# Kernel optimization log

Hardware: AMD Instinct MI355X
Metric: run time of the kernel (lower is better)

## Reference

```python
import jax, jax.numpy as jnp
import numpy as np

N, D, E, H, K = 16384, 1024, 16, 4096, 2


def setup_inputs() -> dict:
    key = jax.random.key(0)
    ks = jax.random.split(key, 6)
    s = 0.02
    return {
        "x": jax.random.normal(ks[0], (N, D), jnp.float32),
        "Wr": jax.random.normal(ks[1], (D, E), jnp.float32) * s,
        "br": jnp.zeros((E,), jnp.float32),
        "Wn": jax.random.normal(ks[2], (D, E), jnp.float32) * s,
        "bn": jnp.zeros((E,), jnp.float32),
        "W1": jax.random.normal(ks[3], (E, D, H), jnp.float32) * s,
        "b1": jnp.zeros((E, H), jnp.float32),
        "W2": jax.random.normal(ks[4], (E, H, 1), jnp.float32) * s,
        "b2": jnp.zeros((E, 1), jnp.float32),
        "k": K,
    }


def reference(x, Wr, br, Wn, bn, W1, b1, W2, b2, k):
    # Router. NOTE: faithful to source — top-k and scattered values come from
    # noise_logits; logits/noise feed only noisy_logits which is dead (only used
    # as a shape template for the -inf tensor), so the randn noise is omitted.
    noise_logits = x @ Wn + bn                      # [N, E]
    vals, idx = jax.lax.top_k(noise_logits, k)      # [N, k]
    # softmax over sparse(-inf filled) logits == softmax over top-k values,
    # scattered back; non-selected experts get exactly 0.
    probs = jax.nn.softmax(vals, axis=-1)           # [N, k]
    n = x.shape[0]
    gates = jnp.zeros((n, noise_logits.shape[-1]), x.dtype)
    gates = gates.at[jnp.arange(n)[:, None], idx].set(probs)  # [N, E]

    # Dense loop over ALL experts (as in source), masked-weighted sum.
    def step(acc, per_expert):
        w1, bb1, w2, bb2, g = per_expert
        h = jax.nn.relu(x @ w1 + bb1)               # [N, H]
        out = h @ w2 + bb2                          # [N, 1]
        return acc + out * g[:, None], None

    init = jnp.zeros((n, 1), x.dtype)
    final_out, _ = jax.lax.scan(step, init, (W1, b1, W2, b2, gates.T))
    return final_out
```

## Files before the change

kernel.cpp:

```cpp
#include <hip/hip_runtime.h>
#include <stdint.h>

#define N_TOK 16384
#define DIM   1024
#define NEXP  16
#define HID   4096

typedef unsigned short ushort_t;
typedef __bf16 bf16x8 __attribute__((ext_vector_type(8)));
typedef float  f32x4  __attribute__((ext_vector_type(4)));
typedef ushort_t u16x8 __attribute__((ext_vector_type(8)));

__device__ __forceinline__ ushort_t f2bf(float f) {
    union { float f; unsigned int u; } v; v.f = f;
    unsigned int r = v.u + 0x7fffu + ((v.u >> 16) & 1u);
    return (ushort_t)(r >> 16);
}

__device__ __forceinline__ void gl_lds16(const void* g, void* l) {
    __builtin_amdgcn_global_load_lds(
        (const __attribute__((address_space(1))) void*)g,
        (__attribute__((address_space(3))) void*)l, 16, 0, 0);
}

#define TS 72
__global__ void __launch_bounds__(256) transpose_w1_kernel(const float* __restrict__ W1,
                                                           ushort_t* __restrict__ w1t) {
    __shared__ ushort_t tileT[64 * TS];
    const int e  = blockIdx.z;
    const int h0 = blockIdx.x * 256;
    const int d0 = blockIdx.y * 64;
    const int t  = threadIdx.x;
    const int hs = t & 15;
    const int dg = t >> 4;
    const float* src = W1 + (size_t)e * DIM * HID;
    float4 rows[4][4];
#pragma unroll
    for (int i = 0; i < 4; ++i) {
        const float* rp = src + (size_t)(d0 + dg * 4 + i) * HID + h0 + hs * 4;
#pragma unroll
        for (int ii = 0; ii < 4; ++ii)
            rows[ii][i] = *(const float4*)(rp + ii * 64);
    }
    ushort_t* dst = w1t + (size_t)e * HID * DIM;
#pragma unroll
    for (int ii = 0; ii < 4; ++ii) {
        if (ii) __syncthreads();
#pragma unroll
        for (int j = 0; j < 4; ++j) {
            float v0 = (&rows[ii][0].x)[j], v1 = (&rows[ii][1].x)[j];
            float v2 = (&rows[ii][2].x)[j], v3 = (&rows[ii][3].x)[j];
            ushort4 col; col.x = f2bf(v0); col.y = f2bf(v1); col.z = f2bf(v2); col.w = f2bf(v3);
            *(ushort4*)&tileT[(hs * 4 + j) * TS + dg * 4] = col;
        }
        __syncthreads();
#pragma unroll
        for (int p = 0; p < 2; ++p) {
            int r = p * 32 + (t >> 3);
            int c = t & 7;
            u16x8 fr = *(const u16x8*)&tileT[r * TS + c * 8];
            *(u16x8*)(dst + (size_t)(h0 + ii * 64 + r) * DIM + d0 + c * 8) = fr;
        }
    }
}

__global__ void __launch_bounds__(256) router_logits_kernel(
    const float* __restrict__ x, const float* __restrict__ Wn,
    const float* __restrict__ bn, const float* __restrict__ b2,
    ushort_t* __restrict__ xbf, int2* __restrict__ eidx,
    float2* __restrict__ probs, float* __restrict__ out) {
    int wave  = threadIdx.x >> 6;
    int lane  = threadIdx.x & 63;
    int token = blockIdx.x * 4 + wave;
    const float* xr = x + (size_t)token * DIM;
    float acc[NEXP];
#pragma unroll
    for (int e = 0; e < NEXP; ++e) acc[e] = 0.f;
    ushort_t xl[16];
#pragma unroll
    for (int i = 0; i < 16; ++i) {
        int d = lane + i * 64;
        float xv = xr[d];
        xl[i] = f2bf(xv);
        const float4* wr = (const float4*)(Wn + d * NEXP);
        float4 w0 = wr[0], w1 = wr[1], w2 = wr[2], w3 = wr[3];
        acc[0]  += xv * w0.x; acc[1]  += xv * w0.y; acc[2]  += xv * w0.z; acc[3]  += xv * w0.w;
        acc[4]  += xv * w1.x; acc[5]  += xv * w1.y; acc[6]  += xv * w1.z; acc[7]  += xv * w1.w;
        acc[8]  += xv * w2.x; acc[9]  += xv * w2.y; acc[10] += xv * w2.z; acc[11] += xv * w2.w;
        acc[12] += xv * w3.x; acc[13] += xv * w3.y; acc[14] += xv * w3.z; acc[15] += xv * w3.w;
    }
    ushort_t* xbr = xbf + (size_t)token * DIM;
#pragma unroll
    for (int i = 0; i < 16; ++i) xbr[lane + i * 64] = xl[i];
#pragma unroll
    for (int e = 0; e < NEXP; ++e) {
        float v = acc[e];
#pragma unroll
        for (int off = 32; off > 0; off >>= 1) v += __shfl_xor(v, off, 64);
        acc[e] = v + bn[e];
    }
    if (lane == 0) {
        float m0 = -1e30f; int i0 = 0;
        for (int e = 0; e < NEXP; ++e) if (acc[e] > m0) { m0 = acc[e]; i0 = e; }
        float m1 = -1e30f; int i1 = 0;
        for (int e = 0; e < NEXP; ++e) if (e != i0 && acc[e] > m1) { m1 = acc[e]; i1 = e; }
        float tq = expf(m1 - m0);
        float p0 = 1.f / (1.f + tq);
        float p1 = 1.f - p0;
        eidx[token]  = make_int2(i0, i1);
        probs[token] = make_float2(p0, p1);
        out[token]   = p0 * b2[i0] + p1 * b2[i1];
    }
}

#define NCHUNK 64
#define CHUNK  (N_TOK / NCHUNK)

__global__ void __launch_bounds__(256) hist_kernel(const int2* __restrict__ eidx,
                                                   int* __restrict__ counts) {
    __shared__ int h[NEXP];
    const int t = threadIdx.x;
    if (t < NEXP) h[t] = 0;
    __syncthreads();
    int token = blockIdx.x * CHUNK + t;
    int2 ei = eidx[token];
    atomicAdd(&h[ei.x], 1);
    atomicAdd(&h[ei.y], 1);
    __syncthreads();
    if (t < NEXP) counts[t * NCHUNK + blockIdx.x] = h[t];
}

__global__ void __launch_bounds__(1024) scan_kernel(const int* __restrict__ counts,
                                                    int* __restrict__ offs,
                                                    int* __restrict__ cnt) {
    const int w    = threadIdx.x >> 6;
    const int lane = threadIdx.x & 63;
    int v = counts[w * NCHUNK + lane];
    int orig = v;
#pragma unroll
    for (int off = 1; off < 64; off <<= 1) {
        int up = __shfl_up(v, off, 64);
        if (lane >= off) v += up;
    }
    offs[w * NCHUNK + lane] = v - orig;
    if (lane == 63) cnt[w] = v;
}

__global__ void __launch_bounds__(256) scatter_kernel(
    const int2* __restrict__ eidx, const float2* __restrict__ probs,
    const int* __restrict__ offs, int* __restrict__ tok, float* __restrict__ gate) {
    __shared__ int wcnt[4][NEXP];
    const int t = threadIdx.x;
    const int wv = t >> 6, lane = t & 63;
    const int token = blockIdx.x * CHUNK + t;
    int2  ei = eidx[token];
    float2 pr = probs[token];
    unsigned long long lmask = (1ull << lane) - 1ull;
#pragma unroll
    for (int e = 0; e < NEXP; ++e) {
        bool s = (ei.x == e) | (ei.y == e);
        unsigned long long m = __ballot(s);
        if (lane == 0) wcnt[wv][e] = __popcll(m);
    }
    __syncthreads();
#pragma unroll
    for (int e = 0; e < NEXP; ++e) {
        bool s0 = (ei.x == e);
        bool s  = s0 | (ei.y == e);
        unsigned long long m = __ballot(s);
        int base = offs[e * NCHUNK + blockIdx.x];
        for (int w = 0; w < wv; ++w) base += wcnt[w][e];
        int pos = base + __popcll(m & lmask);
        if (s) {
            tok[e * N_TOK + pos]  = token;
            gate[e * N_TOK + pos] = s0 ? pr.x : pr.y;
        }
    }
}

__global__ void __launch_bounds__(256, 2) moe_ffn_kernel(
    const ushort_t* __restrict__ xbf, const ushort_t* __restrict__ w1t,
    const float* __restrict__ b1, const float* __restrict__ w2,
    const int* __restrict__ tok, const float* __restrict__ gate,
    const int* __restrict__ cnt, float* __restrict__ out, int eoff) {
    __shared__ ushort_t Alds[128 * 64];
    __shared__ ushort_t Blds[128 * 64];
    const int e  = blockIdx.z + eoff;
    const int ce = cnt[e];
    const int m0 = blockIdx.y * 128;
    if (m0 >= ce) return;
    const int h0 = blockIdx.x * 128;
    const int t    = threadIdx.x;
    const int wv   = t >> 6;
    const int lane = t & 63;
    const int quad = lane >> 4;
    const int ln   = lane & 15;
    const int wm   = (wv >> 1) * 64;
    const int wn   = (wv & 1) * 64;

    int tkid[4];
#pragma unroll
    for (int i = 0; i < 4; ++i) {
        int f = i * 256 + t;
        int r = f >> 3;
        int rr = (m0 + r < ce) ? (m0 + r) : m0;
        tkid[i] = tok[e * N_TOK + rr];
    }

    f32x4 acc[4][4];
    const f32x4 zero = {0.f, 0.f, 0.f, 0.f};
#pragma unroll
    for (int mi = 0; mi < 4; ++mi)
#pragma unroll
        for (int ni = 0; ni < 4; ++ni) acc[mi][ni] = zero;

    for (int k0 = 0; k0 < DIM; k0 += 64) {
#pragma unroll
        for (int i = 0; i < 4; ++i) {
            int f = i * 256 + t;
            int r = f >> 3, c = f & 7;
            int cs = (c ^ (r & 7)) << 3;
            const ushort_t* ga = xbf + (size_t)tkid[i] * DIM + k0 + cs;
            gl_lds16(ga, &Alds[f * 8]);
            const ushort_t* gb = w1t + ((size_t)e * HID + h0 + r) * DIM + k0 + cs;
            gl_lds16(gb, &Blds[f * 8]);
        }
        __syncthreads();
#pragma unroll
        for (int ks = 0; ks < 2; ++ks) {
            int q = ks * 4 + quad;
            int csw = (q ^ (ln & 7)) << 3;
            bf16x8 af[4], bfr[4];
#pragma unroll
            for (int mi = 0; mi < 4; ++mi)
                af[mi] = *(const bf16x8*)&Alds[(wm + mi * 16 + ln) * 64 + csw];
#pragma unroll
            for (int ni = 0; ni < 4; ++ni)
                bfr[ni] = *(const bf16x8*)&Blds[(wn + ni * 16 + ln) * 64 + csw];
#pragma unroll
            for (int mi = 0; mi < 4; ++mi)
#pragma unroll
                for (int ni = 0; ni < 4; ++ni)
                    acc[mi][ni] = __builtin_amdgcn_mfma_f32_16x16x32_bf16(
                        af[mi], bfr[ni], acc[mi][ni], 0, 0, 0);
        }
        __syncthreads();
    }

#pragma unroll
    for (int mi = 0; mi < 4; ++mi) {
        float part[4] = {0.f, 0.f, 0.f, 0.f};
#pragma unroll
        for (int ni = 0; ni < 4; ++ni) {
            int h = h0 + wn + ni * 16 + ln;
            float bb = b1[e * HID + h];
            float ww = w2[e * HID + h];
#pragma unroll
            for (int rg = 0; rg < 4; ++rg) {
                float v = acc[mi][ni][rg] + bb;
                v = v > 0.f ? v : 0.f;
                part[rg] += v * ww;
            }
        }
#pragma unroll
        for (int rg = 0; rg < 4; ++rg) {
            float v = part[rg];
            v += __shfl_xor(v, 1, 64);
            v += __shfl_xor(v, 2, 64);
            v += __shfl_xor(v, 4, 64);
            v += __shfl_xor(v, 8, 64);
            part[rg] = v;
        }
        if (ln == 0) {
#pragma unroll
            for (int rg = 0; rg < 4; ++rg) {
                int r = m0 + wm + mi * 16 + quad * 4 + rg;
                if (r < ce) {
                    int tk  = tok[e * N_TOK + r];
                    float g = gate[e * N_TOK + r];
                    atomicAdd(&out[tk], g * part[rg]);
                }
            }
        }
    }
}

extern "C" void kernel_launch(void* const* d_in, const int* in_sizes, int n_in,
                              void* d_out, int out_size, void* d_ws, size_t ws_size,
                              hipStream_t stream) {
    (void)in_sizes; (void)n_in; (void)out_size; (void)ws_size;
    const float* x  = (const float*)d_in[0];
    const float* Wn = (const float*)d_in[3];
    const float* bn = (const float*)d_in[4];
    const float* W1 = (const float*)d_in[5];
    const float* b1 = (const float*)d_in[6];
    const float* W2 = (const float*)d_in[7];
    const float* b2 = (const float*)d_in[8];
    float* out = (float*)d_out;

    char* ws = (char*)d_ws;
    ushort_t* xbf = (ushort_t*)ws;
    ushort_t* w1t = (ushort_t*)(ws + (size_t)32 * 1024 * 1024);
    char* p2 = ws + (size_t)160 * 1024 * 1024;
    size_t off = 0;
    int*    tok    = (int*)(p2 + off);    off += (size_t)NEXP * N_TOK * 4;
    float*  gate   = (float*)(p2 + off);  off += (size_t)NEXP * N_TOK * 4;
    int*    cnt    = (int*)(p2 + off);    off += 256;
    int2*   eidx   = (int2*)(p2 + off);   off += (size_t)N_TOK * 8;
    float2* probs  = (float2*)(p2 + off); off += (size_t)N_TOK * 8;
    int*    counts = (int*)(p2 + off);    off += NEXP * NCHUNK * 4;
    int*    offs   = (int*)(p2 + off);    off += NEXP * NCHUNK * 4;

    router_logits_kernel<<<N_TOK / 4, 256, 0, stream>>>(x, Wn, bn, b2, xbf, eidx, probs, out);
    hist_kernel<<<NCHUNK, 256, 0, stream>>>(eidx, counts);
    scan_kernel<<<1, 1024, 0, stream>>>(counts, offs, cnt);
    scatter_kernel<<<NCHUNK, 256, 0, stream>>>(eidx, probs, offs, tok, gate);
    transpose_w1_kernel<<<dim3(HID / 256, DIM / 64, NEXP), 256, 0, stream>>>(W1, w1t);
    moe_ffn_kernel<<<dim3(HID / 128, 64, NEXP / 2), 256, 0, stream>>>(xbf, w1t, b1, W2, tok,
                                                                      gate, cnt, out, 0);
    moe_ffn_kernel<<<dim3(HID / 128, 64, NEXP / 2), 256, 0, stream>>>(xbf, w1t, b1, W2, tok,
                                                                      gate, cnt, out, 8);
}
```

Measured before the change: 870.5 us.

## Merge expert FFN launches with XCD-aware block remap; batch router tokens per wave

The two per-half-expert FFN launches become one grid over all 16 experts. The flat block id is remapped so that blocks dispatched round-robin across the 8 XCDs (fid&7) each get a contiguous slice of work, which keeps the same expert's weights and token tiles in one XCD's L2. Separately, the router kernel now has each wave handle 4 tokens, which amortizes the Wn loads and the shuffle reductions. The cost is more registers in the router (64 accumulators) and an extra selection step when lanes 0-3 pick their token's logits.

```diff
diff --git a/kernel.cpp b/kernel.cpp
--- a/kernel.cpp
+++ b/kernel.cpp
@@ -69,44 +69,60 @@
     const float* __restrict__ bn, const float* __restrict__ b2,
     ushort_t* __restrict__ xbf, int2* __restrict__ eidx,
     float2* __restrict__ probs, float* __restrict__ out) {
-    int wave  = threadIdx.x >> 6;
-    int lane  = threadIdx.x & 63;
-    int token = blockIdx.x * 4 + wave;
-    const float* xr = x + (size_t)token * DIM;
-    float acc[NEXP];
-#pragma unroll
-    for (int e = 0; e < NEXP; ++e) acc[e] = 0.f;
-    ushort_t xl[16];
+    const int wave = threadIdx.x >> 6;
+    const int lane = threadIdx.x & 63;
+    const int t0   = blockIdx.x * 16 + wave * 4;
+    float acc[4][NEXP];
+#pragma unroll
+    for (int tt = 0; tt < 4; ++tt)
+#pragma unroll
+        for (int e = 0; e < NEXP; ++e) acc[tt][e] = 0.f;
+    const float* xr0 = x + (size_t)t0 * DIM;
+    ushort_t* xb0 = xbf + (size_t)t0 * DIM;
 #pragma unroll
     for (int i = 0; i < 16; ++i) {
-        int d = lane + i * 64;
-        float xv = xr[d];
-        xl[i] = f2bf(xv);
+        const int d = lane + i * 64;
         const float4* wr = (const float4*)(Wn + d * NEXP);
         float4 w0 = wr[0], w1 = wr[1], w2 = wr[2], w3 = wr[3];
-        acc[0]  += xv * w0.x; acc[1]  += xv * w0.y; acc[2]  += xv * w0.z; acc[3]  += xv * w0.w;
-        acc[4]  += xv * w1.x; acc[5]  += xv * w1.y; acc[6]  += xv * w1.z; acc[7]  += xv * w1.w;
-        acc[8]  += xv * w2.x; acc[9]  += xv * w2.y; acc[10] += xv * w2.z; acc[11] += xv * w2.w;
-        acc[12] += xv * w3.x; acc[13] += xv * w3.y; acc[14] += xv * w3.z; acc[15] += xv * w3.w;
-    }
-    ushort_t* xbr = xbf + (size_t)token * DIM;
-#pragma unroll
-    for (int i = 0; i < 16; ++i) xbr[lane + i * 64] = xl[i];
-#pragma unroll
-    for (int e = 0; e < NEXP; ++e) {
-        float v = acc[e];
-#pragma unroll
-        for (int off = 32; off > 0; off >>= 1) v += __shfl_xor(v, off, 64);
-        acc[e] = v + bn[e];
-    }
-    if (lane == 0) {
+#pragma unroll
+        for (int tt = 0; tt < 4; ++tt) {
+            float xv = xr0[(size_t)tt * DIM + d];
+            xb0[(size_t)tt * DIM + d] = f2bf(xv);
+            acc[tt][0]  += xv * w0.x; acc[tt][1]  += xv * w0.y;
+            acc[tt][2]  += xv * w0.z; acc[tt][3]  += xv * w0.w;
+            acc[tt][4]  += xv * w1.x; acc[tt][5]  += xv * w1.y;
+            acc[tt][6]  += xv * w1.z; acc[tt][7]  += xv * w1.w;
+            acc[tt][8]  += xv * w2.x; acc[tt][9]  += xv * w2.y;
+            acc[tt][10] += xv * w2.z; acc[tt][11] += xv * w2.w;
+            acc[tt][12] += xv * w3.x; acc[tt][13] += xv * w3.y;
+            acc[tt][14] += xv * w3.z; acc[tt][15] += xv * w3.w;
+        }
+    }
+#pragma unroll
+    for (int off = 32; off > 0; off >>= 1)
+#pragma unroll
+        for (int tt = 0; tt < 4; ++tt)
+#pragma unroll
+            for (int e = 0; e < NEXP; ++e)
+                acc[tt][e] += __shfl_xor(acc[tt][e], off, 64);
+    if (lane < 4) {
+        float a[NEXP];
+#pragma unroll
+        for (int e = 0; e < NEXP; ++e) {
+            float vlo = (lane & 1) ? acc[1][e] : acc[0][e];
+            float vhi = (lane & 1) ? acc[3][e] : acc[2][e];
+            a[e] = ((lane & 2) ? vhi : vlo) + bn[e];
+        }
         float m0 = -1e30f; int i0 = 0;
-        for (int e = 0; e < NEXP; ++e) if (acc[e] > m0) { m0 = acc[e]; i0 = e; }
+#pragma unroll
+        for (int e = 0; e < NEXP; ++e) if (a[e] > m0) { m0 = a[e]; i0 = e; }
         float m1 = -1e30f; int i1 = 0;
-        for (int e = 0; e < NEXP; ++e) if (e != i0 && acc[e] > m1) { m1 = acc[e]; i1 = e; }
+#pragma unroll
+        for (int e = 0; e < NEXP; ++e) if (e != i0 && a[e] > m1) { m1 = a[e]; i1 = e; }
         float tq = expf(m1 - m0);
         float p0 = 1.f / (1.f + tq);
         float p1 = 1.f - p0;
+        const int token = t0 + lane;
         eidx[token]  = make_int2(i0, i1);
         probs[token] = make_float2(p0, p1);
         out[token]   = p0 * b2[i0] + p1 * b2[i1];
@@ -182,14 +198,16 @@
     const ushort_t* __restrict__ xbf, const ushort_t* __restrict__ w1t,
     const float* __restrict__ b1, const float* __restrict__ w2,
     const int* __restrict__ tok, const float* __restrict__ gate,
-    const int* __restrict__ cnt, float* __restrict__ out, int eoff) {
+    const int* __restrict__ cnt, float* __restrict__ out) {
     __shared__ ushort_t Alds[128 * 64];
     __shared__ ushort_t Blds[128 * 64];
-    const int e  = blockIdx.z + eoff;
+    const int fid  = blockIdx.x + 32 * (blockIdx.y + 64 * blockIdx.z);
+    const int work = (fid & 7) * 4096 + (fid >> 3);
+    const int e    = work >> 11;
+    const int m0   = ((work >> 5) & 63) * 128;
+    const int h0   = (work & 31) * 128;
     const int ce = cnt[e];
-    const int m0 = blockIdx.y * 128;
     if (m0 >= ce) return;
-    const int h0 = blockIdx.x * 128;
     const int t    = threadIdx.x;
     const int wv   = t >> 6;
     const int lane = t & 63;
@@ -311,13 +329,11 @@
     int*    counts = (int*)(p2 + off);    off += NEXP * NCHUNK * 4;
     int*    offs   = (int*)(p2 + off);    off += NEXP * NCHUNK * 4;
 
-    router_logits_kernel<<<N_TOK / 4, 256, 0, stream>>>(x, Wn, bn, b2, xbf, eidx, probs, out);
+    router_logits_kernel<<<N_TOK / 16, 256, 0, stream>>>(x, Wn, bn, b2, xbf, eidx, probs, out);
     hist_kernel<<<NCHUNK, 256, 0, stream>>>(eidx, counts);
     scan_kernel<<<1, 1024, 0, stream>>>(counts, offs, cnt);
     scatter_kernel<<<NCHUNK, 256, 0, stream>>>(eidx, probs, offs, tok, gate);
     transpose_w1_kernel<<<dim3(HID / 256, DIM / 64, NEXP), 256, 0, stream>>>(W1, w1t);
-    moe_ffn_kernel<<<dim3(HID / 128, 64, NEXP / 2), 256, 0, stream>>>(xbf, w1t, b1, W2, tok,
-                                                                      gate, cnt, out, 0);
-    moe_ffn_kernel<<<dim3(HID / 128, 64, NEXP / 2), 256, 0, stream>>>(xbf, w1t, b1, W2, tok,
-                                                                      gate, cnt, out, 8);
-}
+    moe_ffn_kernel<<<dim3(HID / 128, 64, NEXP), 256, 0, stream>>>(xbf, w1t, b1, W2, tok,
+                                                                  gate, cnt, out);
+}
```

Result: slower. 1.010 ms (+16.0%).
